# Kernel tuning notes

Measured on AMD Instinct MI355X. Metric: run time of the kernel, lower is better.

Reference implementation:

```python
import jax, jax.numpy as jnp
import numpy as np

B, L, D = 2048, 64, 128
NODES = 512
EPS = 1e-6


def setup_inputs() -> dict:
    key = jax.random.key(0)
    ks = jax.random.split(key, 9)
    src_ids = jax.random.randint(ks[0], (B, L), 0, NODES, dtype=jnp.int32)
    dst_ids = jax.random.randint(ks[1], (B, L), 0, NODES, dtype=jnp.int32)
    src_node_ids = jax.random.randint(ks[2], (B,), 1, NODES, dtype=jnp.int32)
    dst_node_ids = jax.random.randint(ks[3], (B,), 1, NODES, dtype=jnp.int32)
    node_interact_times = 100.0 + jax.random.uniform(ks[4], (B,), jnp.float32)
    src_times = jax.random.uniform(ks[5], (B, L), jnp.float32) * 100.0
    dst_times = jax.random.uniform(ks[6], (B, L), jnp.float32) * 100.0
    W1 = jax.random.normal(ks[7], (1, D), jnp.float32) * 0.5
    b1 = jnp.zeros((D,), jnp.float32)
    W2 = jax.random.normal(ks[8], (D, D), jnp.float32) * (1.0 / np.sqrt(D))
    b2 = jnp.zeros((D,), jnp.float32)
    return dict(src_padded_nodes_neighbor_ids=src_ids,
                dst_padded_nodes_neighbor_ids=dst_ids,
                src_node_ids=src_node_ids, dst_node_ids=dst_node_ids,
                node_interact_times=node_interact_times,
                src_padded_nodes_neighbor_times=src_times,
                dst_padded_nodes_neighbor_times=dst_times,
                W1=W1, b1=b1, W2=W2, b2=b2)


def _group_stats(ids, t):
    # per-position stats of the group sharing the same neighbor id. ids,t: (L,)
    n_pos = ids.shape[0]
    eq = ids[:, None] == ids[None, :]                       # (L,L) group membership
    n = eq.sum(1)                                           # group size at each position
    nf = n.astype(t.dtype)
    tb = jnp.broadcast_to(t[None, :], (n_pos, n_pos))
    tmax = jnp.max(jnp.where(eq, tb, -jnp.inf), axis=1)
    tmin = jnp.min(jnp.where(eq, tb, jnp.inf), axis=1)
    # mean(diff(sorted(ts))) == (max-min)/(n-1)
    avg_iat = jnp.where(n > 1, (tmax - tmin) / jnp.maximum(nf - 1.0, 1.0), 0.0)
    # stable rank of each element inside its own group (order statistic)
    pos = jnp.arange(n_pos)
    before = (t[:, None] < t[None, :]) | ((t[:, None] == t[None, :]) & (pos[:, None] < pos[None, :]))
    rank = jnp.sum(eq & before, axis=0)
    split = n // 2
    sel = eq & (rank[None, :] == split[:, None])            # exactly one per group
    t_split = jnp.sum(jnp.where(sel, tb, 0.0), axis=1)      # sorted(ts)[n//2]
    denom = jnp.maximum(nf - split.astype(t.dtype) - 1.0, 1.0)
    recent_iat = jnp.where(n >= 4, (tmax - t_split) / denom, 0.0)
    valid = ids != 0                                        # dicts skip neighbor id 0
    return nf, jnp.where(valid, avg_iat, 0.0), jnp.where(valid, recent_iat, 0.0)


def _cross_lookup(ids_a, ids_b, vals_b):
    # dict.get(nid, 0.0) over the other side's per-group values (id 0 excluded)
    match = (ids_a[:, None] == ids_b[None, :]) & (ids_b[None, :] != 0)
    idx = jnp.argmax(match, axis=1)
    return jnp.where(match.any(1), vals_b[idx], 0.0)


def _last_time(ids_a, ids_b, t_b):
    # dict comprehension keeps the LAST occurrence's timestamp (id 0 excluded)
    match = (ids_a[:, None] == ids_b[None, :]) & (ids_b[None, :] != 0)
    score = jnp.where(match, jnp.arange(ids_b.shape[0])[None, :], -1)
    li = score.max(1)
    return jnp.where(li >= 0, t_b[jnp.maximum(li, 0)], 0.0)


def _side_features(ids_a, t_a, ids_b, t_b, other_node_id, cur_t,
                   n_a, avg_a, rec_a, avg_b, rec_b, other_first):
    ft = t_a.dtype
    c_self = n_a
    c_other = jnp.sum(ids_a[:, None] == ids_b[None, :], axis=1).astype(ft)
    is_other = (ids_a == other_node_id).astype(ft)
    connects = (c_other > 0).astype(ft)
    freq_asym = jnp.where(c_other > 0, c_self / (c_other + EPS), 0.0)
    rcy_self = cur_t - t_a
    rcy_other = cur_t - _last_time(ids_a, ids_b, t_b)
    temp_asym = jnp.where(rcy_self > EPS, rcy_other / (rcy_self + EPS), 0.0)
    iat_other = _cross_lookup(ids_a, ids_b, avg_b)
    iat_asym = jnp.where(iat_other > EPS, avg_a / (iat_other + EPS), 0.0)
    riat_other = _cross_lookup(ids_a, ids_b, rec_b)
    riat_asym = jnp.where(riat_other > EPS, rec_a / (riat_other + EPS), 0.0)
    if other_first:
        head = [c_other, c_self]
    else:
        head = [c_self, c_other]
    return jnp.stack(head + [is_other, connects, freq_asym, temp_asym, iat_asym, riat_asym], axis=1)


def _per_sample(ids_s, ids_d, sid, did, cur_t, t_s, t_d):
    n_s, avg_s, rec_s = _group_stats(ids_s, t_s)
    n_d, avg_d, rec_d = _group_stats(ids_d, t_d)
    f_src = _side_features(ids_s, t_s, ids_d, t_d, did, cur_t,
                           n_s, avg_s, rec_s, avg_d, rec_d, False)
    f_dst = _side_features(ids_d, t_d, ids_s, t_s, sid, cur_t,
                           n_d, avg_d, rec_d, avg_s, rec_s, True)
    return f_src, f_dst


def _mlp_sum(feats, W1, b1, W2, b2):
    # Linear(1->D) -> ReLU -> Linear(D->D), applied per scalar feature, summed over the 8 features
    h = jax.nn.relu(feats[..., None] * W1[0] + b1)           # [B,L,8,D]
    y = jnp.einsum('blfd,de->blfe', h, W2) + b2
    return y.sum(axis=2)                                      # [B,L,D]


def reference(src_padded_nodes_neighbor_ids, dst_padded_nodes_neighbor_ids,
              src_node_ids, dst_node_ids, node_interact_times,
              src_padded_nodes_neighbor_times, dst_padded_nodes_neighbor_times,
              W1, b1, W2, b2):
    f_src, f_dst = jax.vmap(_per_sample)(
        src_padded_nodes_neighbor_ids, dst_padded_nodes_neighbor_ids,
        src_node_ids, dst_node_ids, node_interact_times,
        src_padded_nodes_neighbor_times, dst_padded_nodes_neighbor_times)
    f_src = jnp.where((src_padded_nodes_neighbor_ids == 0)[..., None], 0.0, f_src)
    f_dst = jnp.where((dst_padded_nodes_neighbor_ids == 0)[..., None], 0.0, f_dst)
    src_path_features = _mlp_sum(f_src, W1, b1, W2, b2)
    dst_path_features = _mlp_sum(f_dst, W1, b1, W2, b2)
    return src_path_features, dst_path_features
```

## Files before the change

kernel.cpp:

```cpp
#include <hip/hip_runtime.h>


#define EPSF 1e-6f
#define LDB 136

typedef __attribute__((ext_vector_type(8))) short bf16x8;
typedef __attribute__((ext_vector_type(4))) float f32x4;

__device__ inline short f2bf(float x) {
    unsigned u = __float_as_uint(x);
    unsigned r = (u + 0x7fffu + ((u >> 16) & 1u)) >> 16;
    return (short)r;
}

__global__ void w2t_prep(const float* __restrict__ W2, short* __restrict__ w2t) {
    const int idx = blockIdx.x * 256 + threadIdx.x;
    const int n = idx >> 7, k = idx & 127;
    w2t[n * 128 + k] = f2bf(W2[k * 128 + n]);
}

template <bool FROMWS>
__launch_bounds__(256, 3)
__global__ void lpe_main(const int* __restrict__ src_ids,
                         const int* __restrict__ dst_ids,
                         const int* __restrict__ src_nid,
                         const int* __restrict__ dst_nid,
                         const float* __restrict__ t_now,
                         const float* __restrict__ src_t,
                         const float* __restrict__ dst_t,
                         const float* __restrict__ W1,
                         const float* __restrict__ b1,
                         const float* __restrict__ W2,
                         const float* __restrict__ b2,
                         const short* __restrict__ w2t,
                         float* __restrict__ out)
{
    __shared__ short W2T[128 * LDB];
    __shared__ int2  s_idt[128];
    __shared__ int   s_n[128];
    __shared__ int   s_rank[128];
    __shared__ float s_avg[128];
    __shared__ float s_rec[128];
    __shared__ float s_feats[128][8];
    __shared__ float s_w1[128];
    __shared__ float s_b1[128];

    const int b   = blockIdx.x;
    const int tid = threadIdx.x;

    int   my_id = 0;  float my_t = 0.f;
    int   n_g = 0;    float tmax_g = 0.f;
    float avg_m = 0.f, rec_m = 0.f;

    if (tid < 128) {
        const int side = tid >> 6, i = tid & 63;
        const int*   idp = side ? dst_ids : src_ids;
        const float* tp  = side ? dst_t   : src_t;
        my_id = idp[b * 64 + i];
        my_t  = tp[b * 64 + i];
        s_idt[tid] = make_int2(my_id, __float_as_int(my_t));
        s_w1[tid]  = W1[tid];
        s_b1[tid]  = b1[tid];
    } else {
        const int t2 = tid - 128;
        if constexpr (FROMWS) {
            for (int u = t2; u < 1024; u += 128) {
                const int n = u >> 4, ku = (u & 15) << 3;
                *(bf16x8*)&W2T[n * LDB + ku] = *(const bf16x8*)&w2t[n * 128 + ku];
            }
        } else {
            for (int u = t2; u < 8192; u += 128) {
                const int k = u >> 7, n = u & 127;
                W2T[n * LDB + k] = f2bf(W2[k * 128 + n]);
            }
        }
    }
    __syncthreads();

    if (tid < 128) {
        const int base = tid & 64, i = tid & 63;
        int n = 0, rank = 0;
        float tmax = -3.4e38f, tmin = 3.4e38f;
        for (int j = 0; j < 64; ++j) {
            const int2 e = s_idt[base + j];
            const float tj = __int_as_float(e.y);
            if (e.x == my_id) {
                ++n;
                tmax = fmaxf(tmax, tj);
                tmin = fminf(tmin, tj);
                if (tj < my_t || (tj == my_t && j < i)) ++rank;
            }
        }
        n_g = n; tmax_g = tmax;
        s_n[tid] = n; s_rank[tid] = rank;
        const float avg = (n > 1) ? (tmax - tmin) / (float)(n - 1) : 0.f;
        avg_m = (my_id != 0) ? avg : 0.f;
        s_avg[tid] = avg_m;
    } else {
        const int t2 = tid - 128;
        if constexpr (FROMWS) {
            for (int u = t2 + 1024; u < 2048; u += 128) {
                const int n = u >> 4, ku = (u & 15) << 3;
                *(bf16x8*)&W2T[n * LDB + ku] = *(const bf16x8*)&w2t[n * 128 + ku];
            }
        } else {
            for (int u = t2 + 8192; u < 16384; u += 128) {
                const int k = u >> 7, n = u & 127;
                W2T[n * LDB + k] = f2bf(W2[k * 128 + n]);
            }
        }
    }
    __syncthreads();

    if (tid < 128) {
        const int base = tid & 64;
        const int split = n_g >> 1;
        float tsplit = 0.f;
        for (int j = 0; j < 64; ++j) {
            const int2 e = s_idt[base + j];
            if (e.x == my_id && s_rank[base + j] == split)
                tsplit = __int_as_float(e.y);
        }
        const float denom = fmaxf((float)(n_g - split - 1), 1.f);
        const float rec = (n_g >= 4) ? (tmax_g - tsplit) / denom : 0.f;
        rec_m = (my_id != 0) ? rec : 0.f;
        s_rec[tid] = rec_m;
    }
    __syncthreads();

    if (tid < 128) {
        const int side  = tid >> 6;
        const int obase = 64 - (tid & 64);
        const float cur = t_now[b];
        const int other_node = side ? src_nid[b] : dst_nid[b];

        int c_other = 0, first_idx = -1;
        float last_t = 0.f;
        for (int j = 0; j < 64; ++j) {
            const int2 e = s_idt[obase + j];
            if (e.x == my_id) {
                ++c_other;
                if (e.x != 0) {
                    last_t = __int_as_float(e.y);
                    if (first_idx < 0) first_idx = j;
                }
            }
        }
        const float c_self = (float)n_g;
        const float co     = (float)c_other;
        const float f_is   = (my_id == other_node) ? 1.f : 0.f;
        const float f_conn = (c_other > 0) ? 1.f : 0.f;
        const float f_freq = (c_other > 0) ? c_self / (co + EPSF) : 0.f;
        const float rcy_s  = cur - my_t;
        const float rcy_o  = cur - last_t;
        const float f_temp = (rcy_s > EPSF) ? rcy_o / (rcy_s + EPSF) : 0.f;
        const float iat_o  = (first_idx >= 0) ? s_avg[obase + first_idx] : 0.f;
        const float f_iat  = (iat_o > EPSF) ? avg_m / (iat_o + EPSF) : 0.f;
        const float riat_o = (first_idx >= 0) ? s_rec[obase + first_idx] : 0.f;
        const float f_riat = (riat_o > EPSF) ? rec_m / (riat_o + EPSF) : 0.f;
        const float m = (my_id != 0) ? 1.f : 0.f;
        s_feats[tid][0] = m * c_self;
        s_feats[tid][1] = m * co;
        s_feats[tid][2] = m * f_is;
        s_feats[tid][3] = m * f_conn;
        s_feats[tid][4] = m * f_freq;
        s_feats[tid][5] = m * f_temp;
        s_feats[tid][6] = m * f_iat;
        s_feats[tid][7] = m * f_riat;
    }
    __syncthreads();

    const int lane = tid & 63, wv = tid >> 6;
    const int quad = lane >> 4, ln = lane & 15;

    f32x4 fx[2][2];
    #pragma unroll
    for (int mi = 0; mi < 2; ++mi) {
        const int row = wv * 32 + mi * 16 + ln;
        fx[mi][0] = *(const f32x4*)&s_feats[row][0];
        fx[mi][1] = *(const f32x4*)&s_feats[row][4];
    }

    f32x4 acc[2][8];
    #pragma unroll
    for (int mi = 0; mi < 2; ++mi)
        #pragma unroll
        for (int et = 0; et < 8; ++et)
            acc[mi][et] = (f32x4){0.f, 0.f, 0.f, 0.f};

    #pragma unroll
    for (int kk = 0; kk < 4; ++kk) {
        const int kof = kk * 32 + quad * 8;
        const f32x4 w1a = *(const f32x4*)&s_w1[kof];
        const f32x4 w1b = *(const f32x4*)&s_w1[kof + 4];
        const f32x4 b1a = *(const f32x4*)&s_b1[kof];
        const f32x4 b1b = *(const f32x4*)&s_b1[kof + 4];
        bf16x8 gf[2];
        #pragma unroll
        for (int mi = 0; mi < 2; ++mi) {
            const f32x4 xa = fx[mi][0], xb = fx[mi][1];
            #pragma unroll
            for (int j = 0; j < 8; ++j) {
                const float w  = (j < 4) ? w1a[j] : w1b[j - 4];
                const float bb = (j < 4) ? b1a[j] : b1b[j - 4];
                float s = fmaxf(fmaf(xa[0], w, bb), 0.f);
                s += fmaxf(fmaf(xa[1], w, bb), 0.f);
                s += fmaxf(fmaf(xa[2], w, bb), 0.f);
                s += fmaxf(fmaf(xa[3], w, bb), 0.f);
                s += fmaxf(fmaf(xb[0], w, bb), 0.f);
                s += fmaxf(fmaf(xb[1], w, bb), 0.f);
                s += fmaxf(fmaf(xb[2], w, bb), 0.f);
                s += fmaxf(fmaf(xb[3], w, bb), 0.f);
                gf[mi][j] = f2bf(s);
            }
        }
        #pragma unroll
        for (int et = 0; et < 8; ++et) {
            const bf16x8 af = *(const bf16x8*)&W2T[(et * 16 + ln) * LDB + kof];
            acc[0][et] = __builtin_amdgcn_mfma_f32_16x16x32_bf16(af, gf[0], acc[0][et], 0, 0, 0);
            acc[1][et] = __builtin_amdgcn_mfma_f32_16x16x32_bf16(af, gf[1], acc[1][et], 0, 0, 0);
        }
    }

    const long side_stride = 2048L * 64L * 128L;
    #pragma unroll
    for (int et = 0; et < 8; ++et) {
        const int e0 = et * 16 + quad * 4;
        const f32x4 bb4 = *(const f32x4*)&b2[e0];
        const f32x4 badd = bb4 * 8.f;
        #pragma unroll
        for (int mi = 0; mi < 2; ++mi) {
            const int row  = wv * 32 + mi * 16 + ln;
            const int side = row >> 6, i = row & 63;
            float* po = out + (long)side * side_stride + ((long)(b * 64 + i)) * 128 + e0;
            *(f32x4*)po = acc[mi][et] + badd;
        }
    }
}

extern "C" void kernel_launch(void* const* d_in, const int* in_sizes, int n_in,
                              void* d_out, int out_size, void* d_ws, size_t ws_size,
                              hipStream_t stream) {
    (void)in_sizes; (void)n_in; (void)out_size;
    const int*   src_ids = (const int*)  d_in[0];
    const int*   dst_ids = (const int*)  d_in[1];
    const int*   src_nid = (const int*)  d_in[2];
    const int*   dst_nid = (const int*)  d_in[3];
    const float* t_now   = (const float*)d_in[4];
    const float* src_t   = (const float*)d_in[5];
    const float* dst_t   = (const float*)d_in[6];
    const float* W1      = (const float*)d_in[7];
    const float* b1      = (const float*)d_in[8];
    const float* W2      = (const float*)d_in[9];
    const float* b2      = (const float*)d_in[10];
    float* out = (float*)d_out;

    if (ws_size >= (size_t)(128 * 128 * 2)) {
        short* w2t = (short*)d_ws;
        w2t_prep<<<64, 256, 0, stream>>>(W2, w2t);
        lpe_main<true><<<2048, 256, 0, stream>>>(src_ids, dst_ids, src_nid, dst_nid,
                                                 t_now, src_t, dst_t, W1, b1, W2, b2,
                                                 w2t, out);
    } else {
        lpe_main<false><<<2048, 256, 0, stream>>>(src_ids, dst_ids, src_nid, dst_nid,
                                                  t_now, src_t, dst_t, W1, b1, W2, b2,
                                                  nullptr, out);
    }
}
```

Baseline: 214.2 us.

## Split fused kernel into feature kernel and MFMA GEMM kernel via workspace

Replaces the single fused kernel with two kernels when the workspace is large enough. The first kernel computes the per-position features and the summed ReLU hidden vectors for two samples per block, writes them to workspace as bf16, and also produces the transposed bf16 W2. The second kernel is a dense MFMA GEMM over all 262144 rows, adding 8×b2. This decouples the irregular feature stage from the GEMM so each can use its own occupancy, at the cost of roughly 64 MB of extra global write and read traffic.

```diff
diff --git a/kernel.cpp b/kernel.cpp
--- a/kernel.cpp
+++ b/kernel.cpp
@@ -9,35 +9,213 @@
 
 __device__ inline short f2bf(float x) {
     unsigned u = __float_as_uint(x);
-    unsigned r = (u + 0x7fffu + ((u >> 16) & 1u)) >> 16;
-    return (short)r;
+    return (short)((u + 0x7fffu + ((u >> 16) & 1u)) >> 16);
 }
 
-__global__ void w2t_prep(const float* __restrict__ W2, short* __restrict__ w2t) {
-    const int idx = blockIdx.x * 256 + threadIdx.x;
-    const int n = idx >> 7, k = idx & 127;
-    w2t[n * 128 + k] = f2bf(W2[k * 128 + n]);
+__launch_bounds__(256, 4)
+__global__ void lpe_feats(const int* __restrict__ src_ids,
+                          const int* __restrict__ dst_ids,
+                          const int* __restrict__ src_nid,
+                          const int* __restrict__ dst_nid,
+                          const float* __restrict__ t_now,
+                          const float* __restrict__ src_t,
+                          const float* __restrict__ dst_t,
+                          const float* __restrict__ W1,
+                          const float* __restrict__ b1,
+                          const float* __restrict__ W2,
+                          short* __restrict__ w2t,
+                          short* __restrict__ gws)
+{
+    __shared__ int2  s_idt[256];
+    __shared__ int   s_rank[256];
+    __shared__ float s_avg[256];
+    __shared__ float s_rec[256];
+    __shared__ float s_w1[128];
+    __shared__ float s_b1[128];
+
+    const int tid = threadIdx.x;
+
+    if (blockIdx.x < 64) {
+        const int idx = blockIdx.x * 256 + tid;
+        const int k = idx >> 7, n = idx & 127;
+        w2t[n * 128 + k] = f2bf(W2[idx]);
+    }
+
+    const int h    = tid >> 7;
+    const int b    = (blockIdx.x << 1) | h;
+    const int t    = tid & 127;
+    const int side = t >> 6;
+    const int i    = tid & 63;
+    const int base = tid & ~63;
+
+    const int*   idp = side ? dst_ids : src_ids;
+    const float* tp  = side ? dst_t   : src_t;
+    const int   my_id = idp[b * 64 + i];
+    const float my_t  = tp[b * 64 + i];
+    s_idt[tid] = make_int2(my_id, __float_as_int(my_t));
+    if (tid < 128) { s_w1[tid] = W1[tid]; s_b1[tid] = b1[tid]; }
+    __syncthreads();
+
+    int n_g = 0, rank = 0;
+    float tmax = -3.4e38f, tmin = 3.4e38f;
+    for (int j = 0; j < 64; ++j) {
+        const int2 e = s_idt[base + j];
+        const float tj = __int_as_float(e.y);
+        if (e.x == my_id) {
+            ++n_g;
+            tmax = fmaxf(tmax, tj);
+            tmin = fminf(tmin, tj);
+            if (tj < my_t || (tj == my_t && j < i)) ++rank;
+        }
+    }
+    s_rank[tid] = rank;
+    const float avg   = (n_g > 1) ? (tmax - tmin) / (float)(n_g - 1) : 0.f;
+    const float avg_m = (my_id != 0) ? avg : 0.f;
+    s_avg[tid] = avg_m;
+    __syncthreads();
+
+    const int split = n_g >> 1;
+    float tsplit = 0.f;
+    for (int j = 0; j < 64; ++j) {
+        const int2 e = s_idt[base + j];
+        if (e.x == my_id && s_rank[base + j] == split)
+            tsplit = __int_as_float(e.y);
+    }
+    const float rec   = (n_g >= 4)
+        ? (tmax - tsplit) / fmaxf((float)(n_g - split - 1), 1.f) : 0.f;
+    const float rec_m = (my_id != 0) ? rec : 0.f;
+    s_rec[tid] = rec_m;
+    __syncthreads();
+
+    const int   obase = base ^ 64;
+    const float cur   = t_now[b];
+    const int other_node = side ? src_nid[b] : dst_nid[b];
+
+    int c_other = 0, first_idx = -1;
+    float last_t = 0.f;
+    for (int j = 0; j < 64; ++j) {
+        const int2 e = s_idt[obase + j];
+        if (e.x == my_id) {
+            ++c_other;
+            if (e.x != 0) { last_t = __int_as_float(e.y); if (first_idx < 0) first_idx = j; }
+        }
+    }
+    const float c_self = (float)n_g;
+    const float co     = (float)c_other;
+    const float m      = (my_id != 0) ? 1.f : 0.f;
+    const float x0 = m * c_self;
+    const float x1 = m * co;
+    const float x2 = m * ((my_id == other_node) ? 1.f : 0.f);
+    const float x3 = m * ((c_other > 0) ? 1.f : 0.f);
+    const float x4 = m * ((c_other > 0) ? c_self / (co + EPSF) : 0.f);
+    const float rcy_s = cur - my_t;
+    const float rcy_o = cur - last_t;
+    const float x5 = m * ((rcy_s > EPSF) ? rcy_o / (rcy_s + EPSF) : 0.f);
+    const float iat_o  = (first_idx >= 0) ? s_avg[obase + first_idx] : 0.f;
+    const float x6 = m * ((iat_o > EPSF) ? avg_m / (iat_o + EPSF) : 0.f);
+    const float riat_o = (first_idx >= 0) ? s_rec[obase + first_idx] : 0.f;
+    const float x7 = m * ((riat_o > EPSF) ? rec_m / (riat_o + EPSF) : 0.f);
+
+    short* gp = gws + ((long)b * 128 + t) * 128;
+    #pragma unroll
+    for (int dc = 0; dc < 8; ++dc) {
+        alignas(16) short buf[16];
+        #pragma unroll
+        for (int u = 0; u < 16; ++u) {
+            const float w  = s_w1[dc * 16 + u];
+            const float bb = s_b1[dc * 16 + u];
+            float s = fmaxf(fmaf(x0, w, bb), 0.f);
+            s += fmaxf(fmaf(x1, w, bb), 0.f);
+            s += fmaxf(fmaf(x2, w, bb), 0.f);
+            s += fmaxf(fmaf(x3, w, bb), 0.f);
+            s += fmaxf(fmaf(x4, w, bb), 0.f);
+            s += fmaxf(fmaf(x5, w, bb), 0.f);
+            s += fmaxf(fmaf(x6, w, bb), 0.f);
+            s += fmaxf(fmaf(x7, w, bb), 0.f);
+            buf[u] = f2bf(s);
+        }
+        *(bf16x8*)&gp[dc * 16]     = *(const bf16x8*)&buf[0];
+        *(bf16x8*)&gp[dc * 16 + 8] = *(const bf16x8*)&buf[8];
+    }
 }
 
-template <bool FROMWS>
 __launch_bounds__(256, 3)
-__global__ void lpe_main(const int* __restrict__ src_ids,
-                         const int* __restrict__ dst_ids,
-                         const int* __restrict__ src_nid,
-                         const int* __restrict__ dst_nid,
-                         const float* __restrict__ t_now,
-                         const float* __restrict__ src_t,
-                         const float* __restrict__ dst_t,
-                         const float* __restrict__ W1,
-                         const float* __restrict__ b1,
-                         const float* __restrict__ W2,
+__global__ void lpe_gemm(const short* __restrict__ w2t,
+                         const short* __restrict__ gws,
                          const float* __restrict__ b2,
-                         const short* __restrict__ w2t,
                          float* __restrict__ out)
 {
     __shared__ short W2T[128 * LDB];
+
+    const int tid = threadIdx.x;
+    #pragma unroll
+    for (int it = 0; it < 8; ++it) {
+        const int fi = it * 256 + tid;
+        const int n = fi >> 4, c = fi & 15;
+        *(bf16x8*)&W2T[n * LDB + c * 8] = *(const bf16x8*)&w2t[n * 128 + c * 8];
+    }
+    __syncthreads();
+
+    const int lane = tid & 63, wv = tid >> 6;
+    const int quad = lane >> 4, ln = lane & 15;
+    const int rbase = blockIdx.x * 256 + wv * 64;
+
+    bf16x8 bf[4][4];
+    #pragma unroll
+    for (int rg = 0; rg < 4; ++rg) {
+        const short* gp = gws + ((long)(rbase + rg * 16 + ln)) * 128;
+        #pragma unroll
+        for (int kk = 0; kk < 4; ++kk)
+            bf[rg][kk] = *(const bf16x8*)&gp[kk * 32 + quad * 8];
+    }
+
+    const long side_stride = 2048L * 64L * 128L;
+    #pragma unroll
+    for (int et = 0; et < 8; ++et) {
+        bf16x8 af[4];
+        #pragma unroll
+        for (int kk = 0; kk < 4; ++kk)
+            af[kk] = *(const bf16x8*)&W2T[(et * 16 + ln) * LDB + kk * 32 + quad * 8];
+
+        f32x4 acc[4];
+        #pragma unroll
+        for (int rg = 0; rg < 4; ++rg) acc[rg] = (f32x4){0.f, 0.f, 0.f, 0.f};
+        #pragma unroll
+        for (int kk = 0; kk < 4; ++kk)
+            #pragma unroll
+            for (int rg = 0; rg < 4; ++rg)
+                acc[rg] = __builtin_amdgcn_mfma_f32_16x16x32_bf16(af[kk], bf[rg][kk], acc[rg], 0, 0, 0);
+
+        const int e0 = et * 16 + quad * 4;
+        const f32x4 bb4 = *(const f32x4*)&b2[e0];
+        const f32x4 badd = bb4 * 8.f;
+        #pragma unroll
+        for (int rg = 0; rg < 4; ++rg) {
+            const int r  = rbase + rg * 16 + ln;
+            const int bq = r >> 7, tq = r & 127;
+            const int sd = tq >> 6, ii = tq & 63;
+            float* po = out + (long)sd * side_stride + ((long)(bq * 64 + ii)) * 128 + e0;
+            *(f32x4*)po = acc[rg] + badd;
+        }
+    }
+}
+
+__launch_bounds__(256, 3)
+__global__ void lpe_fused(const int* __restrict__ src_ids,
+                          const int* __restrict__ dst_ids,
+                          const int* __restrict__ src_nid,
+                          const int* __restrict__ dst_nid,
+                          const float* __restrict__ t_now,
+                          const float* __restrict__ src_t,
+                          const float* __restrict__ dst_t,
+                          const float* __restrict__ W1,
+                          const float* __restrict__ b1,
+                          const float* __restrict__ W2,
+                          const float* __restrict__ b2,
+                          float* __restrict__ out)
+{
+    __shared__ short W2T[128 * LDB];
     __shared__ int2  s_idt[128];
-    __shared__ int   s_n[128];
     __shared__ int   s_rank[128];
     __shared__ float s_avg[128];
     __shared__ float s_rec[128];
@@ -63,16 +241,9 @@
         s_b1[tid]  = b1[tid];
     } else {
         const int t2 = tid - 128;
-        if constexpr (FROMWS) {
-            for (int u = t2; u < 1024; u += 128) {
-                const int n = u >> 4, ku = (u & 15) << 3;
-                *(bf16x8*)&W2T[n * LDB + ku] = *(const bf16x8*)&w2t[n * 128 + ku];
-            }
-        } else {
-            for (int u = t2; u < 8192; u += 128) {
-                const int k = u >> 7, n = u & 127;
-                W2T[n * LDB + k] = f2bf(W2[k * 128 + n]);
-            }
+        for (int u = t2; u < 8192; u += 128) {
+            const int k = u >> 7, n = u & 127;
+            W2T[n * LDB + k] = f2bf(W2[k * 128 + n]);
         }
     }
     __syncthreads();
@@ -92,22 +263,15 @@
             }
         }
         n_g = n; tmax_g = tmax;
-        s_n[tid] = n; s_rank[tid] = rank;
+        s_rank[tid] = rank;
         const float avg = (n > 1) ? (tmax - tmin) / (float)(n - 1) : 0.f;
         avg_m = (my_id != 0) ? avg : 0.f;
         s_avg[tid] = avg_m;
     } else {
         const int t2 = tid - 128;
-        if constexpr (FROMWS) {
-            for (int u = t2 + 1024; u < 2048; u += 128) {
-                const int n = u >> 4, ku = (u & 15) << 3;
-                *(bf16x8*)&W2T[n * LDB + ku] = *(const bf16x8*)&w2t[n * 128 + ku];
-            }
-        } else {
-            for (int u = t2 + 8192; u < 16384; u += 128) {
-                const int k = u >> 7, n = u & 127;
-                W2T[n * LDB + k] = f2bf(W2[k * 128 + n]);
-            }
+        for (int u = t2 + 8192; u < 16384; u += 128) {
+            const int k = u >> 7, n = u & 127;
+            W2T[n * LDB + k] = f2bf(W2[k * 128 + n]);
         }
     }
     __syncthreads();
@@ -255,15 +419,17 @@
     const float* b2      = (const float*)d_in[10];
     float* out = (float*)d_out;
 
-    if (ws_size >= (size_t)(128 * 128 * 2)) {
+    const size_t WS_NEEDED = 32768 + (size_t)262144 * 256;
+    if (ws_size >= WS_NEEDED) {
         short* w2t = (short*)d_ws;
-        w2t_prep<<<64, 256, 0, stream>>>(W2, w2t);
-        lpe_main<true><<<2048, 256, 0, stream>>>(src_ids, dst_ids, src_nid, dst_nid,
-                                                 t_now, src_t, dst_t, W1, b1, W2, b2,
-                                                 w2t, out);
+        short* gws = (short*)d_ws + 16384;
+        lpe_feats<<<1024, 256, 0, stream>>>(src_ids, dst_ids, src_nid, dst_nid,
+                                            t_now, src_t, dst_t, W1, b1, W2,
+                                            w2t, gws);
+        lpe_gemm<<<1024, 256, 0, stream>>>(w2t, gws, b2, out);
     } else {
-        lpe_main<false><<<2048, 256, 0, stream>>>(src_ids, dst_ids, src_nid, dst_nid,
-                                                  t_now, src_t, dst_t, W1, b1, W2, b2,
-                                                  nullptr, out);
+        lpe_fused<<<2048, 256, 0, stream>>>(src_ids, dst_ids, src_nid, dst_nid,
+                                            t_now, src_t, dst_t, W1, b1, W2, b2,
+                                            out);
     }
 }
```

After: 234.1 us. 9.3% more time.
